# Kernel optimization log

Hardware: AMD Instinct MI355X
Metric: run time of the kernel (lower is better)

## Reference

```python
import jax, jax.numpy as jnp
import numpy as np

MAX_POS = 512  # hardcoded max_pos_emb in the module
LN_EPS = 1e-5


def setup_inputs() -> dict:
    key = jax.random.key(0)
    ks = jax.random.split(key, 6)
    bs, n, d = 16, 4000, 1024
    h, dh = 8, 128
    inner = h * dh
    return {
        "x": jax.random.normal(ks[0], (bs, n, d), jnp.float32),
        "ln_w": jnp.ones((d,), jnp.float32),
        "ln_b": jnp.zeros((d,), jnp.float32),
        "Wq": (jax.random.normal(ks[1], (inner, d), jnp.float32) * 0.02),
        "Wkv": (jax.random.normal(ks[2], (2 * inner, d), jnp.float32) * 0.02),
        "Wo": (jax.random.normal(ks[3], (d, inner), jnp.float32) * 0.02),
        "bo": jnp.zeros((d,), jnp.float32),
        "rel_emb": (jax.random.normal(ks[4], (2 * MAX_POS + 1, dh), jnp.float32) * 0.02),
        "context_size": 256,
    }


def reference(x, ln_w, ln_b, Wq, Wkv, Wo, bo, rel_emb, context_size):
    bs, n, d = x.shape
    dh = rel_emb.shape[1]
    h = Wq.shape[0] // dh
    scale = dh ** -0.5
    cs = int(context_size)
    nb = -(-n // cs)          # ceil(n / cs)
    nr = n % cs

    # pre_norm (LayerNorm)
    mu = jnp.mean(x, axis=-1, keepdims=True)
    var = jnp.var(x, axis=-1, keepdims=True)
    xn = (x - mu) * jax.lax.rsqrt(var + LN_EPS) * ln_w + ln_b
    if nr > 0:
        xn = jnp.pad(xn, ((0, 0), (0, cs - nr), (0, 0)))

    q = xn @ Wq.T                    # (bs, nb*cs, h*dh)
    k, v = jnp.split(xn @ Wkv.T, 2, axis=-1)

    def blk(t):  # -> (bs, nb, h, cs, dh)
        return t.reshape(bs, nb, cs, h, dh).transpose(0, 1, 3, 2, 4)

    q, k, v = blk(q), blk(k), blk(v)

    # relative position bias, computed as a GEMM instead of broadcast-mul-sum
    seq = jnp.arange(cs)
    dist = jnp.clip(seq[:, None] - seq[None, :], -cs, cs) + MAX_POS
    rel = rel_emb[dist]                                     # (cs, cs, dh)
    pos_attn = jnp.einsum('bnhid,ijd->bnhij', q, rel) * scale

    if nr > 0:
        m = np.ones((cs, cs), dtype=bool)
        m[:nr, :nr] = False
        neg = -jnp.finfo(pos_attn.dtype).max
        pos_attn = pos_attn.at[:, -1].set(
            jnp.where(jnp.asarray(m), neg, pos_attn[:, -1]))

    # SDPA with additive mask: softmax(q k^T * scale + pos_attn) v
    scores = jnp.einsum('bnhid,bnhjd->bnhij', q, k) * scale + pos_attn
    attn = jax.nn.softmax(scores, axis=-1)
    out = jnp.einsum('bnhij,bnhjd->bnhid', attn, v)         # (bs, nb, h, cs, dh)

    out = out.transpose(0, 1, 3, 2, 4).reshape(bs, nb * cs, h * dh)[:, :n]
    return out @ Wo.T + bo  # dropout is identity in eval
```

## Files before the change

kernel.cpp:

```cpp
#include <hip/hip_runtime.h>

typedef __bf16 bf16;
typedef __bf16 bf16x8 __attribute__((ext_vector_type(8)));
typedef float f32x4 __attribute__((ext_vector_type(4)));

#define MFMA16(A,B,C) __builtin_amdgcn_mfma_f32_16x16x32_bf16(A,B,C,0,0,0)
#define SCALE 0.08838834764831843f
#define NEGBIG (-1e30f)

#define AS1(p) ((__attribute__((address_space(1))) void*)(p))
#define AS3(p) ((__attribute__((address_space(3))) void*)(p))

#define BAR() do { asm volatile("" ::: "memory"); __builtin_amdgcn_s_barrier(); asm volatile("" ::: "memory"); } while (0)

__global__ void cvt_bf16(const float* __restrict__ src, bf16* __restrict__ dst, int n) {
    int i = (blockIdx.x * 256 + threadIdx.x) * 4;
    if (i < n) {
        float4 v = *(const float4*)(src + i);
        dst[i + 0] = (bf16)v.x; dst[i + 1] = (bf16)v.y;
        dst[i + 2] = (bf16)v.z; dst[i + 3] = (bf16)v.w;
    }
}

__global__ __launch_bounds__(256) void ln_kernel(const float* __restrict__ x,
                                                 const float* __restrict__ w,
                                                 const float* __restrict__ b,
                                                 bf16* __restrict__ xn) {
    int row = blockIdx.x;
    int bb = row >> 12, p = row & 4095;
    int t = threadIdx.x;
    bf16* out = xn + ((size_t)row << 10);
    if (p >= 4000) {
        uint2 z; z.x = 0u; z.y = 0u;
        *(uint2*)(out + t * 4) = z;
        return;
    }
    float4 v = *(const float4*)(x + (((size_t)bb * 4000 + p) << 10) + t * 4);
    float s = v.x + v.y + v.z + v.w;
    float s2 = v.x * v.x + v.y * v.y + v.z * v.z + v.w * v.w;
#pragma unroll
    for (int m = 1; m < 64; m <<= 1) { s += __shfl_xor(s, m); s2 += __shfl_xor(s2, m); }
    __shared__ float red[8];
    int wv = t >> 6, l = t & 63;
    if (l == 0) { red[wv] = s; red[4 + wv] = s2; }
    __syncthreads();
    s = red[0] + red[1] + red[2] + red[3];
    s2 = red[4] + red[5] + red[6] + red[7];
    float mu = s * (1.f / 1024.f);
    float var = s2 * (1.f / 1024.f) - mu * mu;
    float inv = rsqrtf(var + 1e-5f);
    float4 wv4 = *(const float4*)(w + t * 4);
    float4 bv4 = *(const float4*)(b + t * 4);
    union { bf16 h[4]; uint2 u; } o;
    o.h[0] = (bf16)((v.x - mu) * inv * wv4.x + bv4.x);
    o.h[1] = (bf16)((v.y - mu) * inv * wv4.y + bv4.y);
    o.h[2] = (bf16)((v.z - mu) * inv * wv4.z + bv4.z);
    o.h[3] = (bf16)((v.w - mu) * inv * wv4.w + bv4.w);
    *(uint2*)(out + t * 4) = o.u;
}


__device__ __forceinline__ void stage_half(const bf16* __restrict__ src, int srow, int K,
                                           int kofs, bf16* ldsb, int w, int l) {
#pragma unroll
    for (int r = 0; r < 2; ++r) {
        int rh = (r * 8 + w) * 8 + (l >> 3);
        int chunk = (l & 7) ^ (rh & 7);
        __builtin_amdgcn_global_load_lds(AS1(src + (size_t)(srow + rh) * K + kofs + chunk * 8),
                                         AS3(ldsb + (r * 8 + w) * 512), 16, 0, 0);
    }
}

__device__ __forceinline__ bf16x8 fragLD(const bf16* base, int row, int ks, int lk) {
    int ch = ((ks * 4 + lk) ^ (row & 7)) * 8;
    return *(const bf16x8*)(base + row * 64 + ch);
}

#define RDA(AF, base, mofs) \
    _Pragma("unroll") for (int m = 0; m < 4; ++m) \
    _Pragma("unroll") for (int ks = 0; ks < 2; ++ks) \
        AF[m][ks] = fragLD(base, rA + (mofs + m) * 16 + lrow, ks, lk);

#define RDB2(nb, base) \
    _Pragma("unroll") for (int n = 0; n < 2; ++n) \
    _Pragma("unroll") for (int ks = 0; ks < 2; ++ks) \
        bfr[(nb) + n][ks] = fragLD(base, rB + ((nb) + n) * 16 + lrow, ks, lk);

#define MM(mb, AF, nb) do { \
    __builtin_amdgcn_s_setprio(1); \
    _Pragma("unroll") for (int m = 0; m < 4; ++m) \
    _Pragma("unroll") for (int n = 0; n < 2; ++n) \
    _Pragma("unroll") for (int ks = 0; ks < 2; ++ks) \
        acc[(mb) + m][(nb) + n] = MFMA16(AF[m][ks], bfr[(nb) + n][ks], acc[(mb) + m][(nb) + n]); \
    __builtin_amdgcn_s_setprio(0); } while (0)

template <int EPI>
__global__ __launch_bounds__(512, 2) void gemm256(const bf16* __restrict__ A,
                                                  const bf16* __restrict__ B,
                                                  bf16* __restrict__ C,
                                                  float* __restrict__ Cf,
                                                  const float* __restrict__ bias,
                                                  int M, int N, int K) {
    __shared__ __align__(16) bf16 LA[2 * 16384];
    __shared__ __align__(16) bf16 LB[2 * 16384];
    const int t = threadIdx.x;
    const int w = t >> 6, l = t & 63;
    const int lrow = l & 15, lk = l >> 4;
    const int wrM = w >> 2, wn = w & 3;
    const int rA = wrM * 128, rB = wn * 64;

    const int nwg = gridDim.x, cpx = nwg >> 3;
    const int swz = ((int)blockIdx.x & 7) * cpx + ((int)blockIdx.x >> 3);
    const int nbk = N >> 8;
    const int m0 = (swz / nbk) * 256;
    const int n0 = (swz % nbk) * 256;

    bf16* LA0 = LA;          bf16* LB0 = LB;
    bf16* LA1 = LA + 16384;  bf16* LB1 = LB + 16384;

    f32x4 acc[8][4] = {};
    bf16x8 afL[4][2], afH[4][2], bfr[4][2];

    const int NT = K >> 6, NI = K >> 7;

    stage_half(B, n0,       K, 0,  LB0,        w, l);
    stage_half(B, n0 + 128, K, 0,  LB0 + 8192, w, l);
    stage_half(A, m0,       K, 0,  LA0,        w, l);
    stage_half(A, m0 + 128, K, 0,  LA0 + 8192, w, l);
    stage_half(B, n0,       K, 64, LB1,        w, l);
    stage_half(B, n0 + 128, K, 64, LB1 + 8192, w, l);
    stage_half(A, m0,       K, 64, LA1,        w, l);
    asm volatile("s_waitcnt vmcnt(6)" ::: "memory");
    BAR();

    for (int i = 0; i < NI; ++i) {
        const int kS1 = (2 * i + 1) << 6;
        const int t2 = 2 * i + 2, t3 = 2 * i + 3;
        const int kS2 = ((t2 < NT) ? t2 : NT - 1) << 6;
        const int kS3 = ((t3 < NT) ? t3 : NT - 1) << 6;

        RDA(afL, LA0, 0);
        if (wn < 2) { RDB2(0, LB0); RDB2(2, LB0); } else { RDB2(0, LB0); }
        stage_half(A, m0 + 128, K, kS1, LA1 + 8192, w, l);
        BAR();
        MM(0, afL, 0);
        BAR();
        if (wn >= 2) { RDB2(2, LB0); }
        stage_half(B, n0, K, kS2, LB0, w, l);
        BAR();
        MM(0, afL, 2);
        BAR();
        RDA(afH, LA0, 4);
        stage_half(B, n0 + 128, K, kS2, LB0 + 8192, w, l);
        BAR();
        MM(4, afH, 0);
        BAR();
        stage_half(A, m0, K, kS2, LA0, w, l);
        BAR();
        MM(4, afH, 2);
        asm volatile("s_waitcnt vmcnt(6)" ::: "memory");
        BAR();
        RDA(afL, LA1, 0);
        if (wn < 2) { RDB2(0, LB1); RDB2(2, LB1); } else { RDB2(0, LB1); }
        stage_half(A, m0 + 128, K, kS2, LA0 + 8192, w, l);
        BAR();
        MM(0, afL, 0);
        BAR();
        if (wn >= 2) { RDB2(2, LB1); }
        stage_half(B, n0, K, kS3, LB1, w, l);
        BAR();
        MM(0, afL, 2);
        BAR();
        RDA(afH, LA1, 4);
        stage_half(B, n0 + 128, K, kS3, LB1 + 8192, w, l);
        BAR();
        MM(4, afH, 0);
        BAR();
        stage_half(A, m0, K, kS3, LA1, w, l);
        BAR();
        MM(4, afH, 2);
        asm volatile("s_waitcnt vmcnt(6)" ::: "memory");
        BAR();
    }

    asm volatile("s_waitcnt vmcnt(0)" ::: "memory");

    if (EPI == 0) {
#pragma unroll
        for (int m = 0; m < 8; ++m)
#pragma unroll
            for (int r = 0; r < 4; ++r) {
                size_t row = (size_t)(m0 + rA + m * 16 + lk * 4 + r);
                bf16* dst = C + row * N + n0 + rB;
#pragma unroll
                for (int n = 0; n < 4; ++n) dst[n * 16 + lrow] = (bf16)acc[m][n][r];
            }
    } else {
#pragma unroll
        for (int m = 0; m < 8; ++m)
#pragma unroll
            for (int r = 0; r < 4; ++r) {
                int row = m0 + rA + m * 16 + lk * 4 + r;
                int p = row & 4095, bb2 = row >> 12;
                if (p < 4000) {
                    float* dst = Cf + ((size_t)bb2 * 4000 + p) * 1024 + n0 + rB;
#pragma unroll
                    for (int n = 0; n < 4; ++n)
                        dst[n * 16 + lrow] = acc[m][n][r] + bias[n0 + rB + n * 16 + lrow];
                }
            }
    }
}

__global__ __launch_bounds__(512, 2) void attn_kernel(const bf16* __restrict__ qkv,
                                                      const bf16* __restrict__ relw,
                                                      bf16* __restrict__ ao) {
    int bb = blockIdx.x;
    int h = bb & 7, blkn = (bb >> 3) & 15, b = bb >> 7;
    const int t = threadIdx.x, w = t >> 6, l = t & 63, lrow = l & 15, lk = l >> 4;
    size_t qrow0 = (size_t)(b * 4096 + blkn * 256);
    __shared__ __align__(16) bf16 Ks[64 * 136];
    __shared__ __align__(16) bf16 Vt[128 * 72];
    __shared__ __align__(16) bf16 Wps[8][32 * 96];

    const int i0 = w * 32;
    const bool last = (blkn == 15);
    const int srow = t >> 4, sc8 = t & 15;

    bf16x8 aq[2][4];
#pragma unroll
    for (int mt = 0; mt < 2; ++mt)
#pragma unroll
        for (int ks = 0; ks < 4; ++ks)
            aq[mt][ks] = *(const bf16x8*)(qkv + (qrow0 + i0 + mt * 16 + lrow) * 3072 +
                                          h * 128 + ks * 32 + lk * 8);

    f32x4 o[2][8] = {};
    float mrun[2][4], lrun[2][4];
#pragma unroll
    for (int mt = 0; mt < 2; ++mt)
#pragma unroll
        for (int r = 0; r < 4; ++r) { mrun[mt][r] = NEGBIG; lrun[mt][r] = 0.f; }

    bf16x8 kreg[2], vreg[2];
#pragma unroll
    for (int q = 0; q < 2; ++q) {
        int row = q * 32 + srow;
        kreg[q] = *(const bf16x8*)(qkv + (qrow0 + row) * 3072 + 1024 + h * 128 + sc8 * 8);
        vreg[q] = *(const bf16x8*)(qkv + (qrow0 + row) * 3072 + 2048 + h * 128 + sc8 * 8);
    }
#pragma unroll
    for (int q = 0; q < 2; ++q) {
        int row = q * 32 + srow;
        *(bf16x8*)&Ks[row * 136 + sc8 * 8] = kreg[q];
#pragma unroll
        for (int e = 0; e < 8; ++e) Vt[(sc8 * 8 + e) * 72 + row] = vreg[q][e];
    }
    __syncthreads();

    for (int jt = 0; jt < 4; ++jt) {
        if (jt < 3) {
#pragma unroll
            for (int q = 0; q < 2; ++q) {
                int row = (jt + 1) * 64 + q * 32 + srow;
                kreg[q] = *(const bf16x8*)(qkv + (qrow0 + row) * 3072 + 1024 + h * 128 + sc8 * 8);
                vreg[q] = *(const bf16x8*)(qkv + (qrow0 + row) * 3072 + 2048 + h * 128 + sc8 * 8);
            }
            asm volatile("" ::: "memory");
        }

        f32x4 s[2][4] = {};
#pragma unroll
        for (int nt = 0; nt < 4; ++nt)
#pragma unroll
            for (int ks = 0; ks < 4; ++ks) {
                bf16x8 bk = *(const bf16x8*)&Ks[(nt * 16 + lrow) * 136 + ks * 32 + lk * 8];
                s[0][nt] = MFMA16(aq[0][ks], bk, s[0][nt]);
                s[1][nt] = MFMA16(aq[1][ks], bk, s[1][nt]);
            }

        const int cbase = i0 - jt * 64 + 192;
        f32x4 wacc[2][6] = {};
#pragma unroll
        for (int ks = 0; ks < 4; ++ks)
#pragma unroll
            for (int ct = 0; ct < 6; ++ct) {
                bf16x8 br = *(const bf16x8*)(relw + (size_t)(cbase + ct * 16 + lrow) * 128 +
                                             ks * 32 + lk * 8);
                wacc[0][ct] = MFMA16(aq[0][ks], br, wacc[0][ct]);
                wacc[1][ct] = MFMA16(aq[1][ks], br, wacc[1][ct]);
            }
        bf16* wb = &Wps[w][0];
#pragma unroll
        for (int mt = 0; mt < 2; ++mt)
#pragma unroll
            for (int ct = 0; ct < 6; ++ct)
#pragma unroll
                for (int r = 0; r < 4; ++r)
                    wb[(mt * 16 + lk * 4 + r) * 96 + ct * 16 + lrow] = (bf16)wacc[mt][ct][r];

        float sv[2][4][4];
#pragma unroll
        for (int mt = 0; mt < 2; ++mt)
#pragma unroll
            for (int nt = 0; nt < 4; ++nt)
#pragma unroll
                for (int r = 0; r < 4; ++r) {
                    int row = mt * 16 + lk * 4 + r;
                    int cc = row - nt * 16 - lrow + 63;
                    float xv = (s[mt][nt][r] + (float)wb[row * 96 + cc]) * SCALE;
                    if (last && (i0 + row >= 160 || jt * 64 + nt * 16 + lrow >= 160))
                        xv = NEGBIG;
                    sv[mt][nt][r] = xv;
                }

#pragma unroll
        for (int mt = 0; mt < 2; ++mt)
#pragma unroll
            for (int r = 0; r < 4; ++r) {
                float mx = fmaxf(fmaxf(sv[mt][0][r], sv[mt][1][r]),
                                 fmaxf(sv[mt][2][r], sv[mt][3][r]));
#pragma unroll
                for (int d = 1; d < 16; d <<= 1) mx = fmaxf(mx, __shfl_xor(mx, d));
                float mold = mrun[mt][r];
                float mn = fmaxf(mold, mx);
                float corr = __expf(mold - mn);
                mrun[mt][r] = mn;
                float rs = 0.f;
#pragma unroll
                for (int nt = 0; nt < 4; ++nt) {
                    float e = __expf(sv[mt][nt][r] - mn);
                    sv[mt][nt][r] = e; rs += e;
                }
#pragma unroll
                for (int d = 1; d < 16; d <<= 1) rs += __shfl_xor(rs, d);
                lrun[mt][r] = lrun[mt][r] * corr + rs;
#pragma unroll
                for (int dt = 0; dt < 8; ++dt) o[mt][dt][r] *= corr;
            }

        bf16* ps = &Wps[w][0];
#pragma unroll
        for (int mt = 0; mt < 2; ++mt)
#pragma unroll
            for (int nt = 0; nt < 4; ++nt)
#pragma unroll
                for (int r = 0; r < 4; ++r)
                    ps[(mt * 16 + lk * 4 + r) * 72 + nt * 16 + lrow] = (bf16)sv[mt][nt][r];

#pragma unroll
        for (int pks = 0; pks < 2; ++pks) {
            bf16x8 ap0 = *(const bf16x8*)&ps[lrow * 72 + pks * 32 + lk * 8];
            bf16x8 ap1 = *(const bf16x8*)&ps[(16 + lrow) * 72 + pks * 32 + lk * 8];
#pragma unroll
            for (int dt = 0; dt < 8; ++dt) {
                bf16x8 bv = *(const bf16x8*)&Vt[(dt * 16 + lrow) * 72 + pks * 32 + lk * 8];
                o[0][dt] = MFMA16(ap0, bv, o[0][dt]);
                o[1][dt] = MFMA16(ap1, bv, o[1][dt]);
            }
        }

        __syncthreads();
        if (jt < 3) {
#pragma unroll
            for (int q = 0; q < 2; ++q) {
                int row = q * 32 + srow;
                *(bf16x8*)&Ks[row * 136 + sc8 * 8] = kreg[q];
#pragma unroll
                for (int e = 0; e < 8; ++e) Vt[(sc8 * 8 + e) * 72 + row] = vreg[q][e];
            }
        }
        __syncthreads();
    }

#pragma unroll
    for (int mt = 0; mt < 2; ++mt)
#pragma unroll
        for (int r = 0; r < 4; ++r) {
            float inv = 1.0f / lrun[mt][r];
            size_t arow = qrow0 + i0 + mt * 16 + lk * 4 + r;
            bf16* dst = ao + arow * 1024 + h * 128;
#pragma unroll
            for (int dt = 0; dt < 8; ++dt)
                dst[dt * 16 + lrow] = (bf16)(o[mt][dt][r] * inv);
        }
}

extern "C" void kernel_launch(void* const* d_in, const int* in_sizes, int n_in,
                              void* d_out, int out_size, void* d_ws, size_t ws_size,
                              hipStream_t stream) {
    const float* x   = (const float*)d_in[0];
    const float* lnw = (const float*)d_in[1];
    const float* lnb = (const float*)d_in[2];
    const float* Wq  = (const float*)d_in[3];
    const float* Wkv = (const float*)d_in[4];
    const float* Wo  = (const float*)d_in[5];
    const float* bo  = (const float*)d_in[6];
    const float* rel = (const float*)d_in[7];

    const size_t OFF_XN   = 0;
    const size_t OFF_QKV  = OFF_XN + 134217728ULL;
    const size_t OFF_WCAT = OFF_QKV + 402653184ULL;
    const size_t OFF_WO   = OFF_WCAT + 6291456ULL;
    const size_t OFF_RELW = OFF_WO + 2097152ULL;
    const size_t NEED     = OFF_RELW + 131072ULL;
    if (ws_size < NEED) return;

    char* ws = (char*)d_ws;
    bf16* xn   = (bf16*)(ws + OFF_XN);
    bf16* qkv  = (bf16*)(ws + OFF_QKV);
    bf16* wcat = (bf16*)(ws + OFF_WCAT);
    bf16* wo   = (bf16*)(ws + OFF_WO);
    bf16* relw = (bf16*)(ws + OFF_RELW);
    bf16* ao   = xn;
    float* out = (float*)d_out;

    cvt_bf16<<<1024, 256, 0, stream>>>(Wq, wcat, 1048576);
    cvt_bf16<<<2048, 256, 0, stream>>>(Wkv, wcat + 1048576, 2097152);
    cvt_bf16<<<1024, 256, 0, stream>>>(Wo, wo, 1048576);
    cvt_bf16<<<64, 256, 0, stream>>>(rel + 257 * 128, relw, 65536);
    ln_kernel<<<65536, 256, 0, stream>>>(x, lnw, lnb, xn);
    gemm256<0><<<3072, 512, 0, stream>>>(xn, wcat, qkv, nullptr, nullptr, 65536, 3072, 1024);
    attn_kernel<<<2048, 512, 0, stream>>>(qkv, relw, ao);
    gemm256<1><<<1024, 512, 0, stream>>>(ao, wo, nullptr, out, bo, 65536, 1024, 1024);
}
```

Baseline: 1.234 ms.

## Shift rel-pos bias via ds_permute, swizzle V transpose, raise attention occupancy

The relative-position GEMM results are no longer written to an LDS scratch tile and read back. Each lane instead packs pairs of bf16 values and redistributes them across lanes with ds_permute to apply the diagonal shift. This shrinks the per-warp shared buffer and drops the separate score array. The transposed V tile in LDS now uses an XOR swizzle to reduce bank conflicts on both its scattered writes and vector reads. The launch bound minimum blocks is raised from 2 to 4, which tightens the register budget and risks spills.

```diff
diff --git a/kernel.cpp b/kernel.cpp
--- a/kernel.cpp
+++ b/kernel.cpp
@@ -212,7 +212,7 @@
     }
 }
 
-__global__ __launch_bounds__(512, 2) void attn_kernel(const bf16* __restrict__ qkv,
+__global__ __launch_bounds__(512, 4) void attn_kernel(const bf16* __restrict__ qkv,
                                                       const bf16* __restrict__ relw,
                                                       bf16* __restrict__ ao) {
     int bb = blockIdx.x;
@@ -221,7 +221,7 @@
     size_t qrow0 = (size_t)(b * 4096 + blkn * 256);
     __shared__ __align__(16) bf16 Ks[64 * 136];
     __shared__ __align__(16) bf16 Vt[128 * 72];
-    __shared__ __align__(16) bf16 Wps[8][32 * 96];
+    __shared__ __align__(16) bf16 Ps[8][32 * 72];
 
     const int i0 = w * 32;
     const bool last = (blkn == 15);
@@ -254,9 +254,14 @@
         int row = q * 32 + srow;
         *(bf16x8*)&Ks[row * 136 + sc8 * 8] = kreg[q];
 #pragma unroll
-        for (int e = 0; e < 8; ++e) Vt[(sc8 * 8 + e) * 72 + row] = vreg[q][e];
+        for (int e = 0; e < 8; ++e) {
+            int d = sc8 * 8 + e;
+            Vt[d * 72 + ((((row >> 3) ^ (sc8 & 7)) << 3) | (row & 7))] = vreg[q][e];
+        }
     }
     __syncthreads();
+
+    const int g0 = lk * 4 + 63 - lrow;
 
     for (int jt = 0; jt < 4; ++jt) {
         if (jt < 3) {
@@ -290,36 +295,42 @@
                 wacc[0][ct] = MFMA16(aq[0][ks], br, wacc[0][ct]);
                 wacc[1][ct] = MFMA16(aq[1][ks], br, wacc[1][ct]);
             }
-        bf16* wb = &Wps[w][0];
+
 #pragma unroll
         for (int mt = 0; mt < 2; ++mt)
 #pragma unroll
-            for (int ct = 0; ct < 6; ++ct)
-#pragma unroll
-                for (int r = 0; r < 4; ++r)
-                    wb[(mt * 16 + lk * 4 + r) * 96 + ct * 16 + lrow] = (bf16)wacc[mt][ct][r];
-
-        float sv[2][4][4];
+            for (int r = 0; r < 4; ++r) {
+                const int Kb = g0 + mt * 16 + r;
+                const int dst = ((l & 48) | (Kb & 15)) << 2;
+                unsigned pk[3];
+#pragma unroll
+                for (int P = 0; P < 3; ++P) {
+                    unsigned lo = (unsigned)__builtin_bit_cast(unsigned short,
+                                        (bf16)wacc[mt][2 * P][r]);
+                    unsigned hi = (unsigned)__builtin_bit_cast(unsigned short,
+                                        (bf16)wacc[mt][2 * P + 1][r]);
+                    pk[P] = (unsigned)__builtin_amdgcn_ds_permute(dst, (int)((hi << 16) | lo));
+                }
+#pragma unroll
+                for (int nt = 0; nt < 4; ++nt) {
+                    int bcc = Kb - 16 * nt;
+                    unsigned rec = (bcc < 32) ? pk[0] : (bcc < 64) ? pk[1] : pk[2];
+                    unsigned b16v = ((bcc >> 4) & 1) ? (rec >> 16) : (rec & 0xffffu);
+                    float wvf = __builtin_bit_cast(float, b16v << 16);
+                    float xv = (s[mt][nt][r] + wvf) * SCALE;
+                    if (last && (i0 + mt * 16 + lk * 4 + r >= 160 ||
+                                 jt * 64 + nt * 16 + lrow >= 160))
+                        xv = NEGBIG;
+                    s[mt][nt][r] = xv;
+                }
+            }
+
 #pragma unroll
         for (int mt = 0; mt < 2; ++mt)
 #pragma unroll
-            for (int nt = 0; nt < 4; ++nt)
-#pragma unroll
-                for (int r = 0; r < 4; ++r) {
-                    int row = mt * 16 + lk * 4 + r;
-                    int cc = row - nt * 16 - lrow + 63;
-                    float xv = (s[mt][nt][r] + (float)wb[row * 96 + cc]) * SCALE;
-                    if (last && (i0 + row >= 160 || jt * 64 + nt * 16 + lrow >= 160))
-                        xv = NEGBIG;
-                    sv[mt][nt][r] = xv;
-                }
-
-#pragma unroll
-        for (int mt = 0; mt < 2; ++mt)
-#pragma unroll
             for (int r = 0; r < 4; ++r) {
-                float mx = fmaxf(fmaxf(sv[mt][0][r], sv[mt][1][r]),
-                                 fmaxf(sv[mt][2][r], sv[mt][3][r]));
+                float mx = fmaxf(fmaxf(s[mt][0][r], s[mt][1][r]),
+                                 fmaxf(s[mt][2][r], s[mt][3][r]));
 #pragma unroll
                 for (int d = 1; d < 16; d <<= 1) mx = fmaxf(mx, __shfl_xor(mx, d));
                 float mold = mrun[mt][r];
@@ -329,8 +340,8 @@
                 float rs = 0.f;
 #pragma unroll
                 for (int nt = 0; nt < 4; ++nt) {
-                    float e = __expf(sv[mt][nt][r] - mn);
-                    sv[mt][nt][r] = e; rs += e;
+                    float e = __expf(s[mt][nt][r] - mn);
+                    s[mt][nt][r] = e; rs += e;
                 }
 #pragma unroll
                 for (int d = 1; d < 16; d <<= 1) rs += __shfl_xor(rs, d);
@@ -339,14 +350,14 @@
                 for (int dt = 0; dt < 8; ++dt) o[mt][dt][r] *= corr;
             }
 
-        bf16* ps = &Wps[w][0];
+        bf16* ps = &Ps[w][0];
 #pragma unroll
         for (int mt = 0; mt < 2; ++mt)
 #pragma unroll
             for (int nt = 0; nt < 4; ++nt)
 #pragma unroll
                 for (int r = 0; r < 4; ++r)
-                    ps[(mt * 16 + lk * 4 + r) * 72 + nt * 16 + lrow] = (bf16)sv[mt][nt][r];
+                    ps[(mt * 16 + lk * 4 + r) * 72 + nt * 16 + lrow] = (bf16)s[mt][nt][r];
 
 #pragma unroll
         for (int pks = 0; pks < 2; ++pks) {
@@ -354,7 +365,9 @@
             bf16x8 ap1 = *(const bf16x8*)&ps[(16 + lrow) * 72 + pks * 32 + lk * 8];
 #pragma unroll
             for (int dt = 0; dt < 8; ++dt) {
-                bf16x8 bv = *(const bf16x8*)&Vt[(dt * 16 + lrow) * 72 + pks * 32 + lk * 8];
+                int d = dt * 16 + lrow;
+                int j8 = (pks * 4 + lk) ^ ((d >> 3) & 7);
+                bf16x8 bv = *(const bf16x8*)&Vt[d * 72 + (j8 << 3)];
                 o[0][dt] = MFMA16(ap0, bv, o[0][dt]);
                 o[1][dt] = MFMA16(ap1, bv, o[1][dt]);
             }
@@ -367,7 +380,10 @@
                 int row = q * 32 + srow;
                 *(bf16x8*)&Ks[row * 136 + sc8 * 8] = kreg[q];
 #pragma unroll
-                for (int e = 0; e < 8; ++e) Vt[(sc8 * 8 + e) * 72 + row] = vreg[q][e];
+                for (int e = 0; e < 8; ++e) {
+                    int d = sc8 * 8 + e;
+                    Vt[d * 72 + ((((row >> 3) ^ (sc8 & 7)) << 3) | (row & 7))] = vreg[q][e];
+                }
             }
         }
         __syncthreads();
```

New measurement: 1.732 ms. +40.3%, slower.
